# Performance work log

Measured on AMD Instinct MI355X. Metric: run time of the kernel, lower is better.

## Reference

```python
import jax, jax.numpy as jnp
import numpy as np

N = 100_000      # nodes
E = 1_600_000    # edges (before self-loops)
IN_C = 500
HID = 128
OUT_C = 64
L = 8
ALPHA = 0.1
THETA = 0.5


def setup_inputs() -> dict:
    key = jax.random.key(0)
    ks = jax.random.split(key, 6)
    x = jax.random.normal(ks[0], (N, IN_C), dtype=jnp.float32)
    edge_index = jax.random.randint(ks[1], (2, E), 0, N, dtype=jnp.int32)
    s0 = 1.0 / np.sqrt(IN_C)
    W_in = jax.random.uniform(ks[2], (IN_C, HID), jnp.float32, -s0, s0)
    b_in = jnp.zeros((HID,), jnp.float32)
    sh = 1.0 / np.sqrt(HID)
    W_conv = jax.random.uniform(ks[3], (L, HID, HID), jnp.float32, -sh, sh)
    W_out = jax.random.uniform(ks[4], (HID, OUT_C), jnp.float32, -sh, sh)
    b_out = jnp.zeros((OUT_C,), jnp.float32)
    return {"x": x, "edge_index": edge_index, "W_in": W_in, "b_in": b_in,
            "W_conv": W_conv, "W_out": W_out, "b_out": b_out}


def reference(x, edge_index, W_in, b_in, W_conv, W_out, b_out):
    # dropout is identity in eval mode
    loop = jnp.arange(N, dtype=edge_index.dtype)
    src = jnp.concatenate([edge_index[0], loop])  # add self-loops (gcn_norm)
    dst = jnp.concatenate([edge_index[1], loop])
    deg = jax.ops.segment_sum(jnp.ones_like(src, dtype=x.dtype), dst, num_segments=N)
    dinv = jnp.where(deg > 0, jax.lax.rsqrt(deg), 0.0)
    norm = dinv[src] * dinv[dst]  # symmetric normalization coeffs per edge

    h = jax.nn.relu(x @ W_in + b_in)
    h0 = h  # initial residual
    for l in range(L):
        beta = float(np.log(THETA / (l + 1) + 1.0))
        agg = jax.ops.segment_sum(h[src] * norm[:, None], dst, num_segments=N)  # Ahat @ h
        z = (1.0 - ALPHA) * agg + ALPHA * h0
        h = jax.nn.relu((1.0 - beta) * z + beta * (z @ W_conv[l]))
    return h @ W_out + b_out
```

## Files before the change

kernel.cpp:

```cpp
#include <hip/hip_runtime.h>
#include <hip/hip_fp16.h>
#include <cmath>

#define NN 100000
#define EE 1600000
#define INC 500
#define HIDC 128
#define OUTC 64
#define NLAYER 8
#define NB16 6250
#define NPX 12500
#define GEMM_BLKS 782
#define CNT_BLKS 50000
#define CG_BLKS (GEMM_BLKS + CNT_BLKS)

typedef float f32x4 __attribute__((ext_vector_type(4)));
typedef __bf16 bf16x8 __attribute__((ext_vector_type(8)));
typedef _Float16 f16x8 __attribute__((ext_vector_type(8)));
typedef short s16x4 __attribute__((ext_vector_type(4)));
typedef short s16x8 __attribute__((ext_vector_type(8)));

__device__ __forceinline__ unsigned short f2bf_rn(float f) {
  unsigned u = __float_as_uint(f);
  unsigned r = u + 0x7fffu + ((u >> 16) & 1u);
  return (unsigned short)(r >> 16);
}
__device__ __forceinline__ float bf2f(unsigned short h) {
  return __uint_as_float(((unsigned)h) << 16);
}

__device__ __forceinline__ int fraddr(int row, int k, int Kp) {
  return (row >> 4) * (Kp * 16) + (k >> 3) * 128 + (row & 15) * 8 + (k & 7);
}


__global__ void k_scan_block_sums(const int* __restrict__ deg, int* __restrict__ bsum, int n) {
  __shared__ int sm[256];
  int i = blockIdx.x * 256 + threadIdx.x;
  int v = (i < n) ? deg[i] + 1 : 0;
  sm[threadIdx.x] = v;
  __syncthreads();
  for (int s = 128; s > 0; s >>= 1) {
    if (threadIdx.x < s) sm[threadIdx.x] += sm[threadIdx.x + s];
    __syncthreads();
  }
  if (threadIdx.x == 0) bsum[blockIdx.x] = sm[0];
}

__global__ void k_scan_partials(int* __restrict__ bsum, int nb) {
  __shared__ int sm[512];
  int t = threadIdx.x;
  sm[t] = (t < nb) ? bsum[t] : 0;
  __syncthreads();
  for (int s = 1; s < 512; s <<= 1) {
    int v = (t >= s) ? sm[t - s] : 0;
    __syncthreads();
    sm[t] += v;
    __syncthreads();
  }
  if (t < nb) bsum[t] = (t == 0) ? 0 : sm[t - 1];
}

__global__ void k_scan_final(const int* __restrict__ deg, const int* __restrict__ bsum,
                             int* __restrict__ row_ptr, int n) {
  __shared__ int sm[256];
  int i = blockIdx.x * 256 + threadIdx.x;
  int v = (i < n) ? deg[i] + 1 : 0;
  sm[threadIdx.x] = v;
  __syncthreads();
  for (int s = 1; s < 256; s <<= 1) {
    int u = (threadIdx.x >= s) ? sm[threadIdx.x - s] : 0;
    __syncthreads();
    sm[threadIdx.x] += u;
    __syncthreads();
  }
  if (i < n) row_ptr[i] = bsum[blockIdx.x] + sm[threadIdx.x] - v;
}

__global__ void k_init_rows(const int* __restrict__ deg, const int* __restrict__ row_ptr,
                            int* __restrict__ cursor, int* __restrict__ col,
                            float* __restrict__ dinv, int n) {
  int i = blockIdx.x * blockDim.x + threadIdx.x;
  if (i < n) {
    int rp = row_ptr[i];
    col[rp] = i;
    cursor[i] = rp + 1;
    dinv[i] = rsqrtf((float)(deg[i] + 1));
  }
}

__global__ void __launch_bounds__(256) k_scale(
    const __half* __restrict__ hu, const float* __restrict__ dinv,
    __half* __restrict__ hsc) {
  int i = blockIdx.x * 256 + threadIdx.x;
  int gr = i >> 4, part = i & 15;
  if (gr >= NN) return;
  float dv = dinv[gr];
  s16x8 v = *reinterpret_cast<const s16x8*>(&hu[(size_t)gr * HIDC + part * 8]);
  const __half2* vp = reinterpret_cast<const __half2*>(&v);
  f16x8 w;
#pragma unroll
  for (int j = 0; j < 4; ++j) {
    float2 f = __half22float2(vp[j]);
    w[2 * j]     = (_Float16)(f.x * dv);
    w[2 * j + 1] = (_Float16)(f.y * dv);
  }
  *reinterpret_cast<f16x8*>(&hsc[(size_t)gr * HIDC + part * 8]) = w;
}

__global__ void __launch_bounds__(256) k_fill_x(
    const int* __restrict__ src, const int* __restrict__ dst,
    int* __restrict__ cursor, int* __restrict__ col) {
  int chunk = blockIdx.x >> 3;
  int xcd = blockIdx.x & 7;
  int e = chunk * 256 + threadIdx.x;
  int d = dst[e];
  if (d / NPX == xcd) {
    int pos = atomicAdd(&cursor[d], 1);
    col[pos] = src[e];
  }
}


__global__ void k_prep_wfin(const float* __restrict__ W, unsigned short* __restrict__ fh,
                            unsigned short* __restrict__ fl) {
  int i = blockIdx.x * 256 + threadIdx.x;
  if (i >= HIDC * 512) return;
  int n = i / 512, k = i % 512;
  float v = (k < INC) ? W[(size_t)k * HIDC + n] : 0.f;
  unsigned short h = f2bf_rn(v);
  unsigned short l = f2bf_rn(v - bf2f(h));
  int a = fraddr(n, k, 512);
  fh[a] = h;
  fl[a] = l;
}


__global__ void k_prep_wf16(const float* __restrict__ W, __half* __restrict__ f,
                            int K, int N, float idc, float ws) {
  int i = blockIdx.x * 256 + threadIdx.x;
  if (i >= N * K) return;
  int n = i / K, k = i % K;
  float v = ws * W[(size_t)k * N + n] + ((k == n) ? idc : 0.f);
  f[fraddr(n, k, K)] = __float2half(v);
}


__global__ void __launch_bounds__(256) k_count_gemm(
    const int* __restrict__ dst, int* __restrict__ deg,
    const float* __restrict__ A, const unsigned short* __restrict__ Bfh,
    const unsigned short* __restrict__ Bfl, const float* __restrict__ bias,
    __half* __restrict__ C16u) {
  __shared__ __align__(16) unsigned short Ah[128 * 40];
  __shared__ __align__(16) unsigned short Al[128 * 40];
  int bid = blockIdx.x;
  int tid = threadIdx.x;

  if (bid >= GEMM_BLKS) {
    int o = bid - GEMM_BLKS;
    int chunk = o >> 3;
    int xcd = bid & 7;
    int e = chunk * 256 + tid;
    int d = dst[e];
    if (d / NPX == xcd) atomicAdd(&deg[d], 1);
    return;
  }

  int blk = bid;
  int wid = tid >> 6, lane = tid & 63;
  int wr = wid >> 1, wc = wid & 1;
  int lr = lane & 15, kg = lane >> 4;
  int row0 = blk * 128;

  f32x4 acc[4][4];
#pragma unroll
  for (int m = 0; m < 4; ++m)
#pragma unroll
    for (int n = 0; n < 4; ++n) acc[m][n] = {0.f, 0.f, 0.f, 0.f};

  float4 va[4];
  auto issue_loads = [&](int kt) {
#pragma unroll
    for (int p = 0; p < 4; ++p) {
      int idx = tid + p * 256;
      int r = idx >> 3, kq = idx & 7;
      int gr = row0 + r, gk = kt + kq * 4;
      va[p] = make_float4(0.f, 0.f, 0.f, 0.f);
      if (gr < NN && gk < INC) va[p] = *reinterpret_cast<const float4*>(&A[(size_t)gr * INC + gk]);
    }
  };

  issue_loads(0);
  for (int kt = 0; kt < 512; kt += 32) {
#pragma unroll
    for (int p = 0; p < 4; ++p) {
      int idx = tid + p * 256;
      int r = idx >> 3, kq = idx & 7;
      const float* vp = &va[p].x;
      s16x4 h4, l4;
#pragma unroll
      for (int e = 0; e < 4; ++e) {
        unsigned short h = f2bf_rn(vp[e]);
        h4[e] = (short)h;
        l4[e] = (short)f2bf_rn(vp[e] - bf2f(h));
      }
      *reinterpret_cast<s16x4*>(&Ah[r * 40 + kq * 4]) = h4;
      *reinterpret_cast<s16x4*>(&Al[r * 40 + kq * 4]) = l4;
    }
    __syncthreads();
    if (kt + 32 < 512) issue_loads(kt + 32);

    bf16x8 afh[4], afl[4];
#pragma unroll
    for (int m = 0; m < 4; ++m) {
      int r = wr * 64 + m * 16 + lr;
      afh[m] = *reinterpret_cast<const bf16x8*>(&Ah[r * 40 + kg * 8]);
      afl[m] = *reinterpret_cast<const bf16x8*>(&Al[r * 40 + kg * 8]);
    }
#pragma unroll
    for (int n = 0; n < 4; ++n) {
      size_t bb = (size_t)(wc * 4 + n) * 8192 + (size_t)(kt / 8 + kg) * 128 + lr * 8;
      bf16x8 bh = *reinterpret_cast<const bf16x8*>(&Bfh[bb]);
      bf16x8 bl = *reinterpret_cast<const bf16x8*>(&Bfl[bb]);
#pragma unroll
      for (int m = 0; m < 4; ++m) {
        acc[m][n] = __builtin_amdgcn_mfma_f32_16x16x32_bf16(afh[m], bh, acc[m][n], 0, 0, 0);
        acc[m][n] = __builtin_amdgcn_mfma_f32_16x16x32_bf16(afl[m], bh, acc[m][n], 0, 0, 0);
        acc[m][n] = __builtin_amdgcn_mfma_f32_16x16x32_bf16(afh[m], bl, acc[m][n], 0, 0, 0);
      }
    }
    __syncthreads();
  }

#pragma unroll
  for (int m = 0; m < 4; ++m) {
#pragma unroll
    for (int n = 0; n < 4; ++n) {
      int gc = wc * 64 + n * 16 + lr;
#pragma unroll
      for (int q = 0; q < 4; ++q) {
        int gr = row0 + wr * 64 + m * 16 + kg * 4 + q;
        if (gr < NN) {
          float v = fmaxf(acc[m][n][q] + bias[gc], 0.f);
          C16u[(size_t)gr * HIDC + gc] = __float2half(v);
        }
      }
    }
  }
}


template <int EPI>
__global__ void __launch_bounds__(1024) k_layer(
    const __half* __restrict__ hs, const __half* __restrict__ h0u,
    const __half* __restrict__ Bf,
    const int* __restrict__ row_ptr, const int* __restrict__ deg,
    const int* __restrict__ col, const float* __restrict__ dinv,
    __half* __restrict__ Cs,
    const __half* __restrict__ Bf2, const float* __restrict__ bias2,
    float* __restrict__ outp) {
  __shared__ __half zb[16 * 128];
  int wv = threadIdx.x >> 6, lane = threadIdx.x & 63;
  int g = lane >> 4;
  int fl = lane & 15;
  int row0 = blockIdx.x * 16;
  int node = row0 + wv;

  int start = row_ptr[node];
  int cnt = deg[node] + 1;

  float acc[8];
#pragma unroll
  for (int j = 0; j < 8; ++j) acc[j] = 0.f;

  for (int base = 0; base < cnt; base += 64) {
    int rem = cnt - base;
    if (rem > 64) rem = 64;
    int myc = col[start + base + (lane < rem ? lane : 0)];
    int nch = (rem + 3) >> 2;

    auto get = [&](int ch, s16x8& v, float& m) {
      int e = ch * 4 + g;
      int c = __shfl(myc, e & 63, 64);
      m = (e < rem) ? 1.f : 0.f;
      v = *reinterpret_cast<const s16x8*>(&hs[(size_t)c * HIDC + fl * 8]);
    };

    s16x8 curv; float curm;
    get(0, curv, curm);
    for (int ch = 0; ch < nch; ++ch) {
      s16x8 nv = {}; float nm = 0.f;
      if (ch + 1 < nch) get(ch + 1, nv, nm);
      const __half2* hp = reinterpret_cast<const __half2*>(&curv);
#pragma unroll
      for (int j = 0; j < 4; ++j) {
        float2 f = __half22float2(hp[j]);
        acc[2 * j]     = fmaf(curm, f.x, acc[2 * j]);
        acc[2 * j + 1] = fmaf(curm, f.y, acc[2 * j + 1]);
      }
      curv = nv; curm = nm;
    }
  }

#pragma unroll
  for (int j = 0; j < 8; ++j) {
    acc[j] += __shfl_xor(acc[j], 16, 64);
    acc[j] += __shfl_xor(acc[j], 32, 64);
  }

  if (g == 0) {
    float dr = dinv[node] * 0.9f;
    s16x8 r0 = *reinterpret_cast<const s16x8*>(&h0u[(size_t)node * HIDC + fl * 8]);
    const __half2* r0p = reinterpret_cast<const __half2*>(&r0);
    f16x8 w;
#pragma unroll
    for (int j = 0; j < 4; ++j) {
      float2 f0 = __half22float2(r0p[j]);
      w[2 * j]     = (_Float16)fmaf(dr, acc[2 * j],     0.1f * f0.x);
      w[2 * j + 1] = (_Float16)fmaf(dr, acc[2 * j + 1], 0.1f * f0.y);
    }
    *reinterpret_cast<f16x8*>(&zb[wv * 128 + ((fl * 8) ^ ((wv & 7) << 3))]) = w;
  }
  __syncthreads();

  int lr = lane & 15, kg = lane >> 4;
  f32x4 c = {0.f, 0.f, 0.f, 0.f};
  if (wv < 8) {
    const __half* Bb = Bf + wv * 2048 + kg * 128 + lr * 8;
#pragma unroll
    for (int kt = 0; kt < 4; ++kt) {
      f16x8 a = *reinterpret_cast<const f16x8*>(
          &zb[lr * 128 + ((kt * 32 + kg * 8) ^ ((lr & 7) << 3))]);
      f16x8 b = *reinterpret_cast<const f16x8*>(Bb + kt * 512);
      c = __builtin_amdgcn_mfma_f32_16x16x32_f16(a, b, c, 0, 0, 0);
    }
  }

  if (EPI == 0) {
    if (wv < 8) {
      int gc = wv * 16 + lr;
#pragma unroll
      for (int q = 0; q < 4; ++q) {
        int gr = row0 + kg * 4 + q;
        float v = fmaxf(c[q], 0.f);
        Cs[(size_t)gr * HIDC + gc] = __float2half(v * dinv[gr]);
      }
    }
  } else {
    __syncthreads();
    if (wv < 8) {
      int gc = wv * 16 + lr;
#pragma unroll
      for (int q = 0; q < 4; ++q) {
        int r = kg * 4 + q;
        zb[(gc >> 3) * 128 + r * 8 + (gc & 7)] = __float2half(fmaxf(c[q], 0.f));
      }
    }
    __syncthreads();
    if (wv < 4) {
      f32x4 o = {0.f, 0.f, 0.f, 0.f};
      const __half* Bb2 = Bf2 + wv * 2048 + kg * 128 + lr * 8;
#pragma unroll
      for (int kt = 0; kt < 4; ++kt) {
        f16x8 a = *reinterpret_cast<const f16x8*>(&zb[(kt * 4 + kg) * 128 + lr * 8]);
        f16x8 b = *reinterpret_cast<const f16x8*>(Bb2 + kt * 512);
        o = __builtin_amdgcn_mfma_f32_16x16x32_f16(a, b, o, 0, 0, 0);
      }
      int gc = wv * 16 + lr;
      float bv = bias2[gc];
#pragma unroll
      for (int q = 0; q < 4; ++q) {
        int gr = row0 + kg * 4 + q;
        outp[(size_t)gr * OUTC + gc] = o[q] + bv;
      }
    }
  }
}


extern "C" void kernel_launch(void* const* d_in, const int* in_sizes, int n_in,
                              void* d_out, int out_size, void* d_ws, size_t ws_size,
                              hipStream_t stream) {
  const float* x     = (const float*)d_in[0];
  const int*   ei    = (const int*)d_in[1];
  const float* W_in  = (const float*)d_in[2];
  const float* b_in  = (const float*)d_in[3];
  const float* W_cv  = (const float*)d_in[4];
  const float* W_out = (const float*)d_in[5];
  const float* b_out = (const float*)d_in[6];
  float* out = (float*)d_out;

  char* ws = (char*)d_ws;
  size_t off = 0;
  auto alloc = [&](size_t bytes) {
    char* p = ws + off;
    off = (off + bytes + 255) & ~(size_t)255;
    return p;
  };
  int*    deg     = (int*)alloc((size_t)NN * 4);
  int*    row_ptr = (int*)alloc((size_t)NN * 4);
  int*    cursor  = (int*)alloc((size_t)NN * 4);
  int*    bsum    = (int*)alloc(512 * 4);
  float*  dinv    = (float*)alloc((size_t)NN * 4);
  int*    col     = (int*)alloc((size_t)(EE + NN) * 4);
  __half* h016u   = (__half*)alloc((size_t)NN * HIDC * 2);
  __half* h016s   = (__half*)alloc((size_t)NN * HIDC * 2);
  __half* hsA     = (__half*)alloc((size_t)NN * HIDC * 2);
  __half* hsB     = (__half*)alloc((size_t)NN * HIDC * 2);
  __half* wcv16   = (__half*)alloc((size_t)NLAYER * HIDC * HIDC * 2);
  __half* wout16  = (__half*)alloc((size_t)OUTC * HIDC * 2);
  unsigned short* win_h = (unsigned short*)alloc((size_t)HIDC * 512 * 2);
  unsigned short* win_l = (unsigned short*)alloc((size_t)HIDC * 512 * 2);

  const int* srcp = ei;
  const int* dstp = ei + EE;

  hipMemsetAsync(deg, 0, (size_t)NN * 4, stream);

  k_prep_wfin<<<(HIDC * 512 + 255) / 256, 256, 0, stream>>>(W_in, win_h, win_l);
  for (int l = 0; l < NLAYER; ++l) {
    float beta = logf(0.5f / (float)(l + 1) + 1.0f);
    k_prep_wf16<<<(HIDC * HIDC + 255) / 256, 256, 0, stream>>>(
        W_cv + (size_t)l * HIDC * HIDC, wcv16 + (size_t)l * HIDC * HIDC,
        HIDC, HIDC, 1.0f - beta, beta);
  }
  k_prep_wf16<<<(OUTC * HIDC + 255) / 256, 256, 0, stream>>>(W_out, wout16, HIDC, OUTC,
                                                             0.f, 1.f);

  k_count_gemm<<<CG_BLKS, 256, 0, stream>>>(dstp, deg, x, win_h, win_l, b_in, h016u);

  int nb = (NN + 255) / 256;
  k_scan_block_sums<<<nb, 256, 0, stream>>>(deg, bsum, NN);
  k_scan_partials<<<1, 512, 0, stream>>>(bsum, nb);
  k_scan_final<<<nb, 256, 0, stream>>>(deg, bsum, row_ptr, NN);
  k_init_rows<<<(NN + 255) / 256, 256, 0, stream>>>(deg, row_ptr, cursor, col, dinv, NN);

  k_scale<<<(NN * 16 + 255) / 256, 256, 0, stream>>>(h016u, dinv, h016s);

  k_fill_x<<<CNT_BLKS, 256, 0, stream>>>(srcp, dstp, cursor, col);

  const __half* hcur = h016s;
  for (int l = 0; l < NLAYER; ++l) {
    const __half* wl = wcv16 + (size_t)l * HIDC * HIDC;
    if (l < NLAYER - 1) {
      __half* tgt = (l & 1) ? hsB : hsA;
      k_layer<0><<<NB16, 1024, 0, stream>>>(hcur, h016u, wl, row_ptr, deg, col, dinv,
                                            tgt, nullptr, nullptr, nullptr);
      hcur = tgt;
    } else {
      k_layer<1><<<NB16, 1024, 0, stream>>>(hcur, h016u, wl, row_ptr, deg, col, dinv,
                                            nullptr, wout16, b_out, out);
    }
  }
}
```

Before: 915.5 us.

## Use single fp16 MFMA for input GEMM and fuse it with CSR fill and scaling

```diff
diff --git a/kernel.cpp b/kernel.cpp
--- a/kernel.cpp
+++ b/kernel.cpp
@@ -12,27 +12,26 @@
 #define NPX 12500
 #define GEMM_BLKS 782
 #define CNT_BLKS 50000
-#define CG_BLKS (GEMM_BLKS + CNT_BLKS)
+#define FG_BLKS (GEMM_BLKS + CNT_BLKS)
 
 typedef float f32x4 __attribute__((ext_vector_type(4)));
-typedef __bf16 bf16x8 __attribute__((ext_vector_type(8)));
 typedef _Float16 f16x8 __attribute__((ext_vector_type(8)));
-typedef short s16x4 __attribute__((ext_vector_type(4)));
+typedef _Float16 f16x4 __attribute__((ext_vector_type(4)));
 typedef short s16x8 __attribute__((ext_vector_type(8)));
-
-__device__ __forceinline__ unsigned short f2bf_rn(float f) {
-  unsigned u = __float_as_uint(f);
-  unsigned r = u + 0x7fffu + ((u >> 16) & 1u);
-  return (unsigned short)(r >> 16);
-}
-__device__ __forceinline__ float bf2f(unsigned short h) {
-  return __uint_as_float(((unsigned)h) << 16);
-}
 
 __device__ __forceinline__ int fraddr(int row, int k, int Kp) {
   return (row >> 4) * (Kp * 16) + (k >> 3) * 128 + (row & 15) * 8 + (k & 7);
 }
 
+
+__global__ void __launch_bounds__(256) k_count_x(
+    const int* __restrict__ dst, int* __restrict__ deg) {
+  int chunk = blockIdx.x >> 3;
+  int xcd = blockIdx.x & 7;
+  int e = chunk * 256 + threadIdx.x;
+  int d = dst[e];
+  if (d / NPX == xcd) atomicAdd(&deg[d], 1);
+}
 
 __global__ void k_scan_block_sums(const int* __restrict__ deg, int* __restrict__ bsum, int n) {
   __shared__ int sm[256];
@@ -89,50 +88,13 @@
   }
 }
 
-__global__ void __launch_bounds__(256) k_scale(
-    const __half* __restrict__ hu, const float* __restrict__ dinv,
-    __half* __restrict__ hsc) {
-  int i = blockIdx.x * 256 + threadIdx.x;
-  int gr = i >> 4, part = i & 15;
-  if (gr >= NN) return;
-  float dv = dinv[gr];
-  s16x8 v = *reinterpret_cast<const s16x8*>(&hu[(size_t)gr * HIDC + part * 8]);
-  const __half2* vp = reinterpret_cast<const __half2*>(&v);
-  f16x8 w;
-#pragma unroll
-  for (int j = 0; j < 4; ++j) {
-    float2 f = __half22float2(vp[j]);
-    w[2 * j]     = (_Float16)(f.x * dv);
-    w[2 * j + 1] = (_Float16)(f.y * dv);
-  }
-  *reinterpret_cast<f16x8*>(&hsc[(size_t)gr * HIDC + part * 8]) = w;
-}
-
-__global__ void __launch_bounds__(256) k_fill_x(
-    const int* __restrict__ src, const int* __restrict__ dst,
-    int* __restrict__ cursor, int* __restrict__ col) {
-  int chunk = blockIdx.x >> 3;
-  int xcd = blockIdx.x & 7;
-  int e = chunk * 256 + threadIdx.x;
-  int d = dst[e];
-  if (d / NPX == xcd) {
-    int pos = atomicAdd(&cursor[d], 1);
-    col[pos] = src[e];
-  }
-}
-
-
-__global__ void k_prep_wfin(const float* __restrict__ W, unsigned short* __restrict__ fh,
-                            unsigned short* __restrict__ fl) {
+
+__global__ void k_prep_wfin16(const float* __restrict__ W, __half* __restrict__ f) {
   int i = blockIdx.x * 256 + threadIdx.x;
   if (i >= HIDC * 512) return;
   int n = i / 512, k = i % 512;
   float v = (k < INC) ? W[(size_t)k * HIDC + n] : 0.f;
-  unsigned short h = f2bf_rn(v);
-  unsigned short l = f2bf_rn(v - bf2f(h));
-  int a = fraddr(n, k, 512);
-  fh[a] = h;
-  fl[a] = l;
+  f[fraddr(n, k, 512)] = __float2half(v);
 }
 
 
@@ -146,31 +108,33 @@
 }
 
 
-__global__ void __launch_bounds__(256) k_count_gemm(
-    const int* __restrict__ dst, int* __restrict__ deg,
-    const float* __restrict__ A, const unsigned short* __restrict__ Bfh,
-    const unsigned short* __restrict__ Bfl, const float* __restrict__ bias,
-    __half* __restrict__ C16u) {
-  __shared__ __align__(16) unsigned short Ah[128 * 40];
-  __shared__ __align__(16) unsigned short Al[128 * 40];
+__global__ void __launch_bounds__(256) k_fill_gemm(
+    const int* __restrict__ src, const int* __restrict__ dst,
+    int* __restrict__ cursor, int* __restrict__ col,
+    const float* __restrict__ A, const __half* __restrict__ Bf,
+    const float* __restrict__ bias,
+    __half* __restrict__ C16u, __half* __restrict__ C16s,
+    const float* __restrict__ dinv) {
+  __shared__ __align__(16) _Float16 Ax[128 * 40];
   int bid = blockIdx.x;
   int tid = threadIdx.x;
 
   if (bid >= GEMM_BLKS) {
-    int o = bid - GEMM_BLKS;
-    int chunk = o >> 3;
+    int chunk = (bid - GEMM_BLKS) >> 3;
     int xcd = bid & 7;
     int e = chunk * 256 + tid;
     int d = dst[e];
-    if (d / NPX == xcd) atomicAdd(&deg[d], 1);
+    if (d / NPX == xcd) {
+      int pos = atomicAdd(&cursor[d], 1);
+      col[pos] = src[e];
+    }
     return;
   }
 
-  int blk = bid;
   int wid = tid >> 6, lane = tid & 63;
   int wr = wid >> 1, wc = wid & 1;
   int lr = lane & 15, kg = lane >> 4;
-  int row0 = blk * 128;
+  int row0 = bid * 128;
 
   f32x4 acc[4][4];
 #pragma unroll
@@ -197,37 +161,27 @@
       int idx = tid + p * 256;
       int r = idx >> 3, kq = idx & 7;
       const float* vp = &va[p].x;
-      s16x4 h4, l4;
-#pragma unroll
-      for (int e = 0; e < 4; ++e) {
-        unsigned short h = f2bf_rn(vp[e]);
-        h4[e] = (short)h;
-        l4[e] = (short)f2bf_rn(vp[e] - bf2f(h));
-      }
-      *reinterpret_cast<s16x4*>(&Ah[r * 40 + kq * 4]) = h4;
-      *reinterpret_cast<s16x4*>(&Al[r * 40 + kq * 4]) = l4;
+      f16x4 h4;
+#pragma unroll
+      for (int e = 0; e < 4; ++e) h4[e] = (_Float16)vp[e];
+      *reinterpret_cast<f16x4*>(&Ax[r * 40 + kq * 4]) = h4;
     }
     __syncthreads();
     if (kt + 32 < 512) issue_loads(kt + 32);
 
-    bf16x8 afh[4], afl[4];
+    f16x8 af[4];
 #pragma unroll
     for (int m = 0; m < 4; ++m) {
       int r = wr * 64 + m * 16 + lr;
-      afh[m] = *reinterpret_cast<const bf16x8*>(&Ah[r * 40 + kg * 8]);
-      afl[m] = *reinterpret_cast<const bf16x8*>(&Al[r * 40 + kg * 8]);
+      af[m] = *reinterpret_cast<const f16x8*>(&Ax[r * 40 + kg * 8]);
     }
 #pragma unroll
     for (int n = 0; n < 4; ++n) {
       size_t bb = (size_t)(wc * 4 + n) * 8192 + (size_t)(kt / 8 + kg) * 128 + lr * 8;
-      bf16x8 bh = *reinterpret_cast<const bf16x8*>(&Bfh[bb]);
-      bf16x8 bl = *reinterpret_cast<const bf16x8*>(&Bfl[bb]);
-#pragma unroll
-      for (int m = 0; m < 4; ++m) {
-        acc[m][n] = __builtin_amdgcn_mfma_f32_16x16x32_bf16(afh[m], bh, acc[m][n], 0, 0, 0);
-        acc[m][n] = __builtin_amdgcn_mfma_f32_16x16x32_bf16(afl[m], bh, acc[m][n], 0, 0, 0);
-        acc[m][n] = __builtin_amdgcn_mfma_f32_16x16x32_bf16(afh[m], bl, acc[m][n], 0, 0, 0);
-      }
+      f16x8 b = *reinterpret_cast<const f16x8*>(&Bf[bb]);
+#pragma unroll
+      for (int m = 0; m < 4; ++m)
+        acc[m][n] = __builtin_amdgcn_mfma_f32_16x16x32_f16(af[m], b, acc[m][n], 0, 0, 0);
     }
     __syncthreads();
   }
@@ -243,6 +197,7 @@
         if (gr < NN) {
           float v = fmaxf(acc[m][n][q] + bias[gc], 0.f);
           C16u[(size_t)gr * HIDC + gc] = __float2half(v);
+          C16s[(size_t)gr * HIDC + gc] = __float2half(v * dinv[gr]);
         }
       }
     }
@@ -409,15 +364,14 @@
   __half* hsB     = (__half*)alloc((size_t)NN * HIDC * 2);
   __half* wcv16   = (__half*)alloc((size_t)NLAYER * HIDC * HIDC * 2);
   __half* wout16  = (__half*)alloc((size_t)OUTC * HIDC * 2);
-  unsigned short* win_h = (unsigned short*)alloc((size_t)HIDC * 512 * 2);
-  unsigned short* win_l = (unsigned short*)alloc((size_t)HIDC * 512 * 2);
+  __half* win16   = (__half*)alloc((size_t)HIDC * 512 * 2);
 
   const int* srcp = ei;
   const int* dstp = ei + EE;
 
   hipMemsetAsync(deg, 0, (size_t)NN * 4, stream);
 
-  k_prep_wfin<<<(HIDC * 512 + 255) / 256, 256, 0, stream>>>(W_in, win_h, win_l);
+  k_prep_wfin16<<<(HIDC * 512 + 255) / 256, 256, 0, stream>>>(W_in, win16);
   for (int l = 0; l < NLAYER; ++l) {
     float beta = logf(0.5f / (float)(l + 1) + 1.0f);
     k_prep_wf16<<<(HIDC * HIDC + 255) / 256, 256, 0, stream>>>(
@@ -427,7 +381,7 @@
   k_prep_wf16<<<(OUTC * HIDC + 255) / 256, 256, 0, stream>>>(W_out, wout16, HIDC, OUTC,
                                                              0.f, 1.f);
 
-  k_count_gemm<<<CG_BLKS, 256, 0, stream>>>(dstp, deg, x, win_h, win_l, b_in, h016u);
+  k_count_x<<<CNT_BLKS, 256, 0, stream>>>(dstp, deg);
 
   int nb = (NN + 255) / 256;
   k_scan_block_sums<<<nb, 256, 0, stream>>>(deg, bsum, NN);
@@ -435,9 +389,8 @@
   k_scan_final<<<nb, 256, 0, stream>>>(deg, bsum, row_ptr, NN);
   k_init_rows<<<(NN + 255) / 256, 256, 0, stream>>>(deg, row_ptr, cursor, col, dinv, NN);
 
-  k_scale<<<(NN * 16 + 255) / 256, 256, 0, stream>>>(h016u, dinv, h016s);
-
-  k_fill_x<<<CNT_BLKS, 256, 0, stream>>>(srcp, dstp, cursor, col);
+  k_fill_gemm<<<FG_BLKS, 256, 0, stream>>>(srcp, dstp, cursor, col,
+                                           x, win16, b_in, h016u, h016s, dinv);
 
   const __half* hcur = h016s;
   for (int l = 0; l < NLAYER; ++l) {
```

After: 923.5 us. Within noise of the previous version (+0.9%).
